# Optimization experiments

Measured on AMD Instinct MI355X. Metric: run time of the kernel, lower is better.

Reference implementation:

```python
import jax, jax.numpy as jnp
import numpy as np
import math

N_HEADS = 16
D_HEAD = 64
D_MODEL = 1024
ROPE_THETA = 10000.0


def setup_inputs() -> dict:
    key = jax.random.key(0)
    k1, k2, k3 = jax.random.split(key, 3)
    B, T = 2, 2048
    x = jax.random.normal(k1, (B, T, D_MODEL), dtype=jnp.float32)
    # torch Linear(in, out) weight has shape (out, in); store transposed (in, out)
    # so forward is x @ w. Scale like default init to keep activations sane.
    w_qkv = jax.random.normal(k2, (D_MODEL, 3 * D_MODEL), dtype=jnp.float32) / math.sqrt(D_MODEL)
    w_o = jax.random.normal(k3, (D_MODEL, D_MODEL), dtype=jnp.float32) / math.sqrt(D_MODEL)
    return {"x": x, "w_qkv": w_qkv, "w_o": w_o}


def _build_rope(T, dtype):
    inv_freq = 1.0 / (ROPE_THETA ** (jnp.arange(0, D_HEAD, 2, dtype=jnp.float32) / D_HEAD))
    t = jnp.arange(T, dtype=jnp.float32)
    freqs = jnp.outer(t, inv_freq)            # [T, D_HEAD/2]
    emb = jnp.concatenate([freqs, freqs], -1)  # [T, D_HEAD]
    return jnp.cos(emb).astype(dtype), jnp.sin(emb).astype(dtype)


def _apply_rope(x, cos, sin):
    # x: [B, T, H, D_HEAD]; cos/sin broadcast as [1, T, 1, D_HEAD]
    x1, x2 = jnp.split(x, 2, axis=-1)
    rotated = jnp.concatenate([-x2, x1], axis=-1)
    return x * cos + rotated * sin


def reference(x, w_qkv, w_o):
    B, T, D = x.shape
    qkv = (x @ w_qkv).reshape(B, T, 3, N_HEADS, D_HEAD)
    q, k, v = qkv[:, :, 0], qkv[:, :, 1], qkv[:, :, 2]  # [B, T, H, Dh]
    cos, sin = _build_rope(T, x.dtype)
    cos = cos[None, :, None, :]
    sin = sin[None, :, None, :]
    q = _apply_rope(q, cos, sin)
    k = _apply_rope(k, cos, sin)
    scale = 1.0 / math.sqrt(D_HEAD)
    # full [B, H, T, T] scores (faithful to the manual matmul-softmax-matmul)
    attn = jnp.einsum("bthd,bshd->bhts", q, k) * scale
    attn = jax.nn.softmax(attn, axis=-1)
    out = jnp.einsum("bhts,bshd->bthd", attn, v).reshape(B, T, D)
    return out @ w_o
```

## Files before the change

kernel.cpp:

```cpp
#include <hip/hip_runtime.h>
#include <cstdint>

typedef unsigned short ushort_t;
typedef __attribute__((ext_vector_type(8))) short v8s;
typedef __attribute__((ext_vector_type(4))) short v4s;
typedef __attribute__((ext_vector_type(2))) unsigned v2u;
typedef __attribute__((ext_vector_type(4))) float v4f;

#define MFMA(a, b, c) __builtin_amdgcn_mfma_f32_16x16x32_bf16(a, b, c, 0, 0, 0)
#define QSCALE 0.18033688011112042f

#define GLL(gp, lp) __builtin_amdgcn_global_load_lds(                        \
    (const __attribute__((address_space(1))) void*)(gp),                     \
    (__attribute__((address_space(3))) void*)(lp), 16, 0, 0)

#define WAIT_LGKM0() __builtin_amdgcn_s_waitcnt(0xc07f)

__device__ __forceinline__ float bf2f(ushort_t u) {
    union { unsigned u; float f; } x; x.u = ((unsigned)u) << 16; return x.f;
}
__device__ __forceinline__ short f2bf(float f) {
    union { float f; unsigned u; } x; x.f = f;
    unsigned r = x.u + 0x7fffu + ((x.u >> 16) & 1u);
    return (short)(r >> 16);
}

__global__ __launch_bounds__(256) void prep(const void* __restrict__ xin,
                                            const void* __restrict__ w1,
                                            const void* __restrict__ w2,
                                            ushort_t* __restrict__ xb,
                                            ushort_t* __restrict__ out1,
                                            ushort_t* __restrict__ out2,
                                            int* __restrict__ flag,
                                            float* __restrict__ tab) {
    __shared__ ushort_t tile[64][65];
    __shared__ int cnt;
    int bid = blockIdx.x, tid = threadIdx.x;

    int isbf = 0;
    if (bid < 3072 || bid == 3328) {
        if (tid == 0) cnt = 0;
        __syncthreads();
        unsigned w = ((const unsigned*)xin)[tid];
        int e = (w >> 7) & 0xFF;
        int hit = ((e >= 96 && e <= 135) || (w & 0xFFFFu) == 0) ? 1 : 0;
        atomicAdd(&cnt, hit);
        __syncthreads();
        isbf = (cnt >= 160) ? 1 : 0;
        if (bid == 3328) {
            if (tid == 0) *flag = isbf;
            return;
        }
    }

    if (bid < 2048) {
        int i = bid * 256 + tid;
        if (isbf) {
            ((v8s*)xb)[i] = ((const v8s*)xin)[i];
        } else {
            const float* xf = (const float*)xin + (size_t)i * 8;
            v8s o;
            #pragma unroll
            for (int j = 0; j < 8; ++j) o[j] = f2bf(xf[j]);
            ((v8s*)xb)[i] = o;
        }
    } else if (bid < 3072) {
        int t = bid - 2048;
        int bxl = t & 63, by = (t >> 6) * 64;
        const void* in; ushort_t* out; int C, bx;
        if (bxl < 48) { in = w1; out = out1; C = 3072; bx = bxl * 64; }
        else          { in = w2; out = out2; C = 1024; bx = (bxl - 48) * 64; }
        const int R = 1024;
        int tx = tid & 63, ty = tid >> 6;
        for (int i = ty; i < 64; i += 4) {
            size_t idx = (size_t)(by + i) * C + bx + tx;
            tile[i][tx] = isbf ? ((const ushort_t*)in)[idx]
                               : (ushort_t)f2bf(((const float*)in)[idx]);
        }
        __syncthreads();
        for (int i = ty; i < 64; i += 4) out[(size_t)(bx + i) * R + by + tx] = tile[tx][i];
    } else {
        int idx = (bid - 3072) * 256 + tid;
        int d = idx >> 11, t = idx & 2047;
        float inv_freq = __expf(-(float)d * 0.28782313662425575f);
        float ang = (float)t * inv_freq;
        float sn, cs;
        sincosf(ang, &sn, &cs);
        tab[d * 2048 + t]         = bf2f((ushort_t)f2bf(cs));
        tab[65536 + d * 2048 + t] = bf2f((ushort_t)f2bf(sn));
    }
}

template <int MODE, int BN>
__global__ __launch_bounds__(256) void gemm_bt(const ushort_t* __restrict__ A,
                                               const ushort_t* __restrict__ BT,
                                               void* __restrict__ C,
                                               const int* __restrict__ flagp,
                                               int M, int N, int K,
                                               ushort_t* __restrict__ Qp,
                                               ushort_t* __restrict__ Kp,
                                               ushort_t* __restrict__ Vp,
                                               const float* __restrict__ tab) {
    constexpr int NJ = BN / 32;
    __shared__ __align__(16) ushort_t As[2][128 * 32];
    __shared__ __align__(16) ushort_t Bs[2][BN * 32];
    int tid = threadIdx.x;
    int lane = tid & 63;
    int lr = lane & 15, lc = lane >> 4;
    int w = tid >> 6;
    int wr = (w >> 1) * 64, wc = (w & 1) * (BN / 2);

    int nx = gridDim.x;
    int orig = blockIdx.y * nx + blockIdx.x;
    int cpx = (nx * gridDim.y) >> 3;
    int swz = (orig & 7) * cpx + (orig >> 3);
    int m0 = (swz / nx) * 128, n0 = (swz % nx) * BN;

    int c0 = tid, c1 = tid + 256;
    int r0 = c0 >> 2, s0 = c0 & 3;
    int r1 = c1 >> 2, s1 = c1 & 3;

    const ushort_t* Ag0 = A + (size_t)(m0 + r0) * K + s0 * 8;
    const ushort_t* Ag1 = A + (size_t)(m0 + r1) * K + s1 * 8;
    const ushort_t* Bg0 = BT + (size_t)(n0 + r0) * K + s0 * 8;
    const ushort_t* Bg1 = BT + (size_t)(n0 + r1) * K + s1 * 8;
    const int aoff0 = w * 512;
    const int aoff1 = 2048 + w * 512;
    const int boff0 = w * 512;
    const int boff1 = 2048 + w * 512;

    v4f acc[4][NJ] = {};

    GLL(Ag0, &As[0][aoff0]);
    GLL(Ag1, &As[0][aoff1]);
    GLL(Bg0, &Bs[0][boff0]);
    if constexpr (BN == 128) GLL(Bg1, &Bs[0][boff1]);
    __syncthreads();

    int buf = 0;
    for (int kt = 0; kt < K; kt += 32) {
        if (kt + 32 < K) {
            int nb = buf ^ 1;
            GLL(Ag0 + kt + 32, &As[nb][aoff0]);
            GLL(Ag1 + kt + 32, &As[nb][aoff1]);
            GLL(Bg0 + kt + 32, &Bs[nb][boff0]);
            if constexpr (BN == 128) GLL(Bg1 + kt + 32, &Bs[nb][boff1]);
        }

        v8s af[4], bfr[NJ];
        #pragma unroll
        for (int i = 0; i < 4; ++i)
            af[i] = *(const v8s*)(&As[buf][0] + (wr + i * 16 + lr) * 32 + lc * 8);
        #pragma unroll
        for (int j = 0; j < NJ; ++j)
            bfr[j] = *(const v8s*)(&Bs[buf][0] + (wc + j * 16 + lr) * 32 + lc * 8);
        #pragma unroll
        for (int i = 0; i < 4; ++i)
            #pragma unroll
            for (int j = 0; j < NJ; ++j)
                acc[i][j] = MFMA(af[i], bfr[j], acc[i][j]);

        __syncthreads();
        buf ^= 1;
    }

    if (MODE == 1) {
        int store_f32 = (*flagp == 0);
        #pragma unroll
        for (int i = 0; i < 4; ++i)
            #pragma unroll
            for (int j = 0; j < NJ; ++j)
                #pragma unroll
                for (int r = 0; r < 4; ++r) {
                    int row = m0 + wr + i * 16 + lc * 4 + r;
                    int col = n0 + wc + j * 16 + lr;
                    if (store_f32)
                        ((float*)C)[(size_t)row * N + col] = acc[i][j][r];
                    else
                        ((ushort_t*)C)[(size_t)row * N + col] = (ushort_t)f2bf(acc[i][j][r]);
                }
    } else {
        int region = n0 >> 10;
        int h = ((n0 & 1023) + wc) >> 6;
        if (region < 2) {
            const float sc = (region == 0) ? QSCALE : 1.0f;
            ushort_t* dst = (region == 0) ? Qp : Kp;
            #pragma unroll
            for (int i = 0; i < 4; ++i)
                #pragma unroll
                for (int j = 0; j < 2; ++j) {
                    int d = j * 16 + lr;
                    int tg0 = m0 + wr + i * 16 + lc * 4;
                    int b = tg0 >> 11, tt0 = tg0 & 2047;
                    v4f cs4 = *(const v4f*)(tab + d * 2048 + tt0);
                    v4f sn4 = *(const v4f*)(tab + 65536 + d * 2048 + tt0);
                    #pragma unroll
                    for (int r = 0; r < 4; ++r) {
                        float x1 = acc[i][j][r], x2 = acc[i][(j + 2) % NJ][r];
                        size_t base = ((size_t)(b * 16 + h) * 2048 + tt0 + r) * 64 + d;
                        dst[base]      = (ushort_t)f2bf((x1 * cs4[r] - x2 * sn4[r]) * sc);
                        dst[base + 32] = (ushort_t)f2bf((x2 * cs4[r] + x1 * sn4[r]) * sc);
                    }
                }
        } else {
            #pragma unroll
            for (int i = 0; i < 4; ++i)
                #pragma unroll
                for (int j = 0; j < NJ; ++j) {
                    int d = j * 16 + lr;
                    int tg0 = m0 + wr + i * 16 + lc * 4;
                    int b = tg0 >> 11, tt = tg0 & 2047;
                    v4s pk;
                    #pragma unroll
                    for (int r = 0; r < 4; ++r) pk[r] = f2bf(acc[i][j][r]);
                    size_t base = (size_t)(b * 16 + h) * 131072 + (size_t)(tt >> 5) * 2048
                                + (size_t)d * 32 + (tt & 31);
                    *(v4s*)(Vp + base) = pk;
                }
        }
    }
}

__global__ __launch_bounds__(256) void gemm_o(const ushort_t* __restrict__ A,
                                              const ushort_t* __restrict__ BT,
                                              void* __restrict__ C,
                                              const int* __restrict__ flagp) {
    constexpr int K = 1024, N = 1024;
    __shared__ __align__(16) ushort_t As[2][128 * 64];
    __shared__ __align__(16) ushort_t Bs[2][64 * 64];
    int tid = threadIdx.x;
    int lane = tid & 63;
    int lr = lane & 15, lc = lane >> 4;
    int w = tid >> 6;
    int wr = (w >> 1) * 64, wc = (w & 1) * 32;

    int nx = gridDim.x;
    int orig = blockIdx.y * nx + blockIdx.x;
    int cpx = (nx * gridDim.y) >> 3;
    int swz = (orig & 7) * cpx + (orig >> 3);
    int m0 = (swz / nx) * 128, n0 = (swz % nx) * 64;

    const ushort_t* ag[4]; const ushort_t* bg[2];
    int al[4], bl[2];
    #pragma unroll
    for (int q = 0; q < 4; ++q) {
        int c = q * 256 + tid, r = c >> 3, p = c & 7;
        ag[q] = A + (size_t)(m0 + r) * K + ((p ^ (r & 7)) * 8);
        al[q] = (q * 256 + w * 64) * 8;
    }
    #pragma unroll
    for (int q = 0; q < 2; ++q) {
        int c = q * 256 + tid, r = c >> 3, p = c & 7;
        bg[q] = BT + (size_t)(n0 + r) * K + ((p ^ (r & 7)) * 8);
        bl[q] = (q * 256 + w * 64) * 8;
    }

    v4f acc[4][2] = {};

    #pragma unroll
    for (int q = 0; q < 4; ++q) GLL(ag[q], &As[0][al[q]]);
    #pragma unroll
    for (int q = 0; q < 2; ++q) GLL(bg[q], &Bs[0][bl[q]]);
    __syncthreads();

    int buf = 0;
    for (int t = 0; t < 16; ++t) {
        if (t + 1 < 16) {
            int kg = (t + 1) * 64, nb = buf ^ 1;
            #pragma unroll
            for (int q = 0; q < 4; ++q) GLL(ag[q] + kg, &As[nb][al[q]]);
            #pragma unroll
            for (int q = 0; q < 2; ++q) GLL(bg[q] + kg, &Bs[nb][bl[q]]);
        }

        v8s af[4][2], bf[2][2];
        #pragma unroll
        for (int i = 0; i < 4; ++i)
            #pragma unroll
            for (int kk = 0; kk < 2; ++kk)
                af[i][kk] = *(const v8s*)(&As[buf][0] + (wr + i * 16 + lr) * 64
                                          + (((kk * 4 + lc) ^ (lr & 7)) * 8));
        #pragma unroll
        for (int j = 0; j < 2; ++j)
            #pragma unroll
            for (int kk = 0; kk < 2; ++kk)
                bf[j][kk] = *(const v8s*)(&Bs[buf][0] + (wc + j * 16 + lr) * 64
                                          + (((kk * 4 + lc) ^ (lr & 7)) * 8));
        __builtin_amdgcn_s_setprio(1);
        #pragma unroll
        for (int i = 0; i < 4; ++i)
            #pragma unroll
            for (int j = 0; j < 2; ++j) {
                acc[i][j] = MFMA(af[i][0], bf[j][0], acc[i][j]);
                acc[i][j] = MFMA(af[i][1], bf[j][1], acc[i][j]);
            }
        __builtin_amdgcn_s_setprio(0);

        __syncthreads();
        buf ^= 1;
    }

    int store_f32 = (*flagp == 0);
    #pragma unroll
    for (int i = 0; i < 4; ++i)
        #pragma unroll
        for (int j = 0; j < 2; ++j)
            #pragma unroll
            for (int r = 0; r < 4; ++r) {
                int row = m0 + wr + i * 16 + lc * 4 + r;
                int col = n0 + wc + j * 16 + lr;
                if (store_f32)
                    ((float*)C)[(size_t)row * N + col] = acc[i][j][r];
                else
                    ((ushort_t*)C)[(size_t)row * N + col] = (ushort_t)f2bf(acc[i][j][r]);
            }
}

__global__ __launch_bounds__(512) void attn(const ushort_t* __restrict__ Qr,
                                            const ushort_t* __restrict__ Kr,
                                            const ushort_t* __restrict__ Vt,
                                            ushort_t* __restrict__ AO) {
    __shared__ __align__(16) char lds[65536];
    int tid = threadIdx.x, lane = tid & 63, W = tid >> 6;
    int lr = lane & 15, lc = lane >> 4;
    int qsub = W & 1, sh = W >> 1;
    int L = blockIdx.x;
    int bh = (L & 7) * 4 + ((L >> 3) & 3);
    int qt = L >> 5;
    int q0 = qt * 128 + qsub * 64;
    int b = bh >> 4, h = bh & 15;
    const ushort_t* Qb = Qr + ((size_t)bh * 2048 + q0) * 64;
    const ushort_t* Kb = Kr + (size_t)bh * 131072 + (size_t)sh * 32768;
    const ushort_t* Vb = Vt + (size_t)bh * 131072 + (size_t)sh * 32768;
    ushort_t* KsG = (ushort_t*)(lds + sh * 16384);
    ushort_t* VsG = (ushort_t*)(lds + sh * 16384 + 8192);

    int gt = tid & 127;
    int c0 = gt, c1 = gt + 128;
    int kr0 = c0 >> 3, kc0 = c0 & 7, kr1 = c1 >> 3, kc1 = c1 & 7;
    const ushort_t* Kg0 = Kb + (size_t)kr0 * 64 + kc0 * 8;
    const ushort_t* Kg1 = Kb + (size_t)kr1 * 64 + kc1 * 8;
    int kl0 = kr0 * 64 + (kc0 ^ (kr0 & 7)) * 8;
    int kl1 = kr1 * 64 + (kc1 ^ (kr1 & 7)) * 8;
    const ushort_t* Vg0 = Vb + (size_t)c0 * 8;
    const ushort_t* Vg1 = Vb + (size_t)c1 * 8;
    int vl0 = c0 * 8, vl1 = c1 * 8;

    int blr = (lr >> 2) * 8 + (lr & 3);

    v8s qf[4][2];
    #pragma unroll
    for (int jq = 0; jq < 4; ++jq)
        #pragma unroll
        for (int kk = 0; kk < 2; ++kk)
            qf[jq][kk] = *(const v8s*)(Qb + (size_t)(jq * 16 + lr) * 64 + kk * 32 + lc * 8);

    v4f o[4][4] = {};
    float li[4] = {0.f, 0.f, 0.f, 0.f};

    v8s ka = *(const v8s*)(Kg0), kb2 = *(const v8s*)(Kg1);
    v8s va = *(const v8s*)(Vg0), vb2 = *(const v8s*)(Vg1);
    *(v8s*)(KsG + kl0) = ka;
    *(v8s*)(KsG + kl1) = kb2;
    *(v8s*)(VsG + vl0) = va;
    *(v8s*)(VsG + vl1) = vb2;
    ka  = *(const v8s*)(Kg0 + 2048);
    kb2 = *(const v8s*)(Kg1 + 2048);
    va  = *(const v8s*)(Vg0 + 2048);
    vb2 = *(const v8s*)(Vg1 + 2048);
    __syncthreads();

    #pragma unroll 1
    for (int t = 0; t < 16; ++t) {
        int p = t & 1;
        const ushort_t* Kl = KsG + p * 2048;
        const ushort_t* Vl = VsG + p * 2048;

        v8s kf[2][2], vf[4];
        #pragma unroll
        for (int hh = 0; hh < 2; ++hh) {
            int rn = blr + hh * 4;
            int sw = hh * 4 + (lr & 3);
            #pragma unroll
            for (int kk = 0; kk < 2; ++kk)
                kf[hh][kk] = *(const v8s*)(Kl + rn * 64 + (((kk * 4 + lc) ^ sw) * 8));
        }
        #pragma unroll
        for (int i = 0; i < 4; ++i)
            vf[i] = *(const v8s*)(Vl + (i * 16 + lr) * 32 + lc * 8);

        v4f St[2][4] = {};
        __builtin_amdgcn_s_setprio(1);
        #pragma unroll
        for (int hh = 0; hh < 2; ++hh)
            #pragma unroll
            for (int jq = 0; jq < 4; ++jq) {
                St[hh][jq] = MFMA(kf[hh][0], qf[jq][0], St[hh][jq]);
                St[hh][jq] = MFMA(kf[hh][1], qf[jq][1], St[hh][jq]);
            }
        __builtin_amdgcn_s_setprio(0);

        if (t + 1 < 16) {
            ushort_t* Kn = KsG + (p ^ 1) * 2048;
            ushort_t* Vn = VsG + (p ^ 1) * 2048;
            *(v8s*)(Kn + kl0) = ka;
            *(v8s*)(Kn + kl1) = kb2;
            *(v8s*)(Vn + vl0) = va;
            *(v8s*)(Vn + vl1) = vb2;
        }
        if (t + 2 < 16) {
            ka  = *(const v8s*)(Kg0 + (size_t)(t + 2) * 2048);
            kb2 = *(const v8s*)(Kg1 + (size_t)(t + 2) * 2048);
            va  = *(const v8s*)(Vg0 + (size_t)(t + 2) * 2048);
            vb2 = *(const v8s*)(Vg1 + (size_t)(t + 2) * 2048);
        }

        v8s pf[4];
        #pragma unroll
        for (int jq = 0; jq < 4; ++jq) {
            union { unsigned u[4]; v8s v; } P;
            #pragma unroll
            for (int hh = 0; hh < 2; ++hh) {
                #pragma unroll
                for (int r = 0; r < 4; ++r) {
                    float ev = __builtin_amdgcn_exp2f(St[hh][jq][r]);
                    St[hh][jq][r] = ev;
                    li[jq] += ev;
                }
                P.u[hh * 2 + 0] = __builtin_amdgcn_perm(__float_as_uint(St[hh][jq][1]),
                                                        __float_as_uint(St[hh][jq][0]), 0x07060302u);
                P.u[hh * 2 + 1] = __builtin_amdgcn_perm(__float_as_uint(St[hh][jq][3]),
                                                        __float_as_uint(St[hh][jq][2]), 0x07060302u);
            }
            pf[jq] = P.v;
        }
        __builtin_amdgcn_s_setprio(1);
        #pragma unroll
        for (int jq = 0; jq < 4; ++jq)
            #pragma unroll
            for (int i = 0; i < 4; ++i)
                o[i][jq] = MFMA(vf[i], pf[jq], o[i][jq]);
        __builtin_amdgcn_s_setprio(0);
        WAIT_LGKM0();
        __builtin_amdgcn_s_barrier();
    }

    #pragma unroll
    for (int jq = 0; jq < 4; ++jq) {
        li[jq] += __shfl_xor(li[jq], 16);
        li[jq] += __shfl_xor(li[jq], 32);
    }

    float* MO = (float*)lds;
    float* Ml = (float*)(lds + 52224);
    __syncthreads();
    #pragma unroll 1
    for (int ph = 0; ph < 2; ++ph) {
        if (qsub == ph && sh != 0) {
            float* M = MO + (sh - 1) * 4352;
            #pragma unroll
            for (int jq = 0; jq < 4; ++jq) {
                #pragma unroll
                for (int i = 0; i < 4; ++i)
                    *(v4f*)(M + (jq * 16 + lr) * 68 + i * 16 + lc * 4) = o[i][jq];
                if (lc == 0) Ml[(sh - 1) * 64 + jq * 16 + lr] = li[jq];
            }
        }
        __syncthreads();
        if (qsub == ph && sh == 0) {
            #pragma unroll
            for (int jq = 0; jq < 4; ++jq) {
                int row = jq * 16 + lr;
                float ls = li[jq] + Ml[row] + Ml[64 + row] + Ml[128 + row];
                float inv = 1.0f / ls;
                int tq = q0 + row;
                #pragma unroll
                for (int i = 0; i < 4; ++i) {
                    v4f m0v = *(const v4f*)(MO + row * 68 + i * 16 + lc * 4);
                    v4f m1v = *(const v4f*)(MO + 4352 + row * 68 + i * 16 + lc * 4);
                    v4f m2v = *(const v4f*)(MO + 8704 + row * 68 + i * 16 + lc * 4);
                    v4s pk;
                    #pragma unroll
                    for (int r = 0; r < 4; ++r)
                        pk[r] = f2bf((o[i][jq][r] + m0v[r] + m1v[r] + m2v[r]) * inv);
                    *(v4s*)(AO + (size_t)(b * 2048 + tq) * 1024 + h * 64 + i * 16 + lc * 4) = pk;
                }
            }
        }
        __syncthreads();
    }
}

extern "C" void kernel_launch(void* const* d_in, const int* in_sizes, int n_in,
                              void* d_out, int out_size, void* d_ws, size_t ws_size,
                              hipStream_t stream) {
    char* ws = (char*)d_ws;
    int*      flag  = (int*)ws;
    ushort_t* wqkvT = (ushort_t*)(ws + 256);
    ushort_t* woT   = (ushort_t*)(ws + 6291712);
    ushort_t* xb    = (ushort_t*)(ws + 8388864);
    ushort_t* Qr    = (ushort_t*)(ws + 16777472);
    ushort_t* Kr    = (ushort_t*)(ws + 25166080);
    ushort_t* Vt    = (ushort_t*)(ws + 33554688);
    ushort_t* AO    = (ushort_t*)(ws + 41943296);
    float*    tab   = (float*)(ws + 50331904);

    prep<<<3329, 256, 0, stream>>>(d_in[0], d_in[1], d_in[2], xb, wqkvT, woT, flag, tab);
    gemm_bt<2, 128><<<dim3(24, 32), 256, 0, stream>>>(xb, wqkvT, nullptr, flag, 4096, 3072, 1024,
                                                      Qr, Kr, Vt, tab);
    attn<<<512, 512, 0, stream>>>(Qr, Kr, Vt, AO);
    gemm_o<<<dim3(16, 32), 256, 0, stream>>>(AO, woT, d_out, flag);
}
```

Baseline: 187.2 us.

## Load V fragments directly from global in attention; shrink output GEMM tile

Attention no longer stages V tiles through LDS. Each wave reads its V fragments directly from global memory every iteration, which cuts LDS use and removes the LDS store/load traffic for V. The output projection GEMM now uses 64x64 tiles with twice as many blocks and a higher occupancy launch bound. The risks are exposed global-load latency for V, since it is no longer prefetched, and less reuse per block in the GEMM.

```diff
diff --git a/kernel.cpp b/kernel.cpp
--- a/kernel.cpp
+++ b/kernel.cpp
@@ -221,46 +221,41 @@
     }
 }
 
-__global__ __launch_bounds__(256) void gemm_o(const ushort_t* __restrict__ A,
-                                              const ushort_t* __restrict__ BT,
-                                              void* __restrict__ C,
-                                              const int* __restrict__ flagp) {
+__global__ __launch_bounds__(256, 4) void gemm_o(const ushort_t* __restrict__ A,
+                                                 const ushort_t* __restrict__ BT,
+                                                 void* __restrict__ C,
+                                                 const int* __restrict__ flagp) {
     constexpr int K = 1024, N = 1024;
-    __shared__ __align__(16) ushort_t As[2][128 * 64];
+    __shared__ __align__(16) ushort_t As[2][64 * 64];
     __shared__ __align__(16) ushort_t Bs[2][64 * 64];
     int tid = threadIdx.x;
     int lane = tid & 63;
     int lr = lane & 15, lc = lane >> 4;
     int w = tid >> 6;
-    int wr = (w >> 1) * 64, wc = (w & 1) * 32;
+    int wr = (w >> 1) * 32, wc = (w & 1) * 32;
 
     int nx = gridDim.x;
     int orig = blockIdx.y * nx + blockIdx.x;
     int cpx = (nx * gridDim.y) >> 3;
     int swz = (orig & 7) * cpx + (orig >> 3);
-    int m0 = (swz / nx) * 128, n0 = (swz % nx) * 64;
-
-    const ushort_t* ag[4]; const ushort_t* bg[2];
-    int al[4], bl[2];
-    #pragma unroll
-    for (int q = 0; q < 4; ++q) {
+    int m0 = (swz / nx) * 64, n0 = (swz % nx) * 64;
+
+    const ushort_t* ag[2]; const ushort_t* bg[2];
+    int lof[2];
+    #pragma unroll
+    for (int q = 0; q < 2; ++q) {
         int c = q * 256 + tid, r = c >> 3, p = c & 7;
         ag[q] = A + (size_t)(m0 + r) * K + ((p ^ (r & 7)) * 8);
-        al[q] = (q * 256 + w * 64) * 8;
-    }
-    #pragma unroll
-    for (int q = 0; q < 2; ++q) {
-        int c = q * 256 + tid, r = c >> 3, p = c & 7;
         bg[q] = BT + (size_t)(n0 + r) * K + ((p ^ (r & 7)) * 8);
-        bl[q] = (q * 256 + w * 64) * 8;
-    }
-
-    v4f acc[4][2] = {};
-
-    #pragma unroll
-    for (int q = 0; q < 4; ++q) GLL(ag[q], &As[0][al[q]]);
-    #pragma unroll
-    for (int q = 0; q < 2; ++q) GLL(bg[q], &Bs[0][bl[q]]);
+        lof[q] = (q * 256 + w * 64) * 8;
+    }
+
+    v4f acc[2][2] = {};
+
+    #pragma unroll
+    for (int q = 0; q < 2; ++q) GLL(ag[q], &As[0][lof[q]]);
+    #pragma unroll
+    for (int q = 0; q < 2; ++q) GLL(bg[q], &Bs[0][lof[q]]);
     __syncthreads();
 
     int buf = 0;
@@ -268,14 +263,14 @@
         if (t + 1 < 16) {
             int kg = (t + 1) * 64, nb = buf ^ 1;
             #pragma unroll
-            for (int q = 0; q < 4; ++q) GLL(ag[q] + kg, &As[nb][al[q]]);
-            #pragma unroll
-            for (int q = 0; q < 2; ++q) GLL(bg[q] + kg, &Bs[nb][bl[q]]);
-        }
-
-        v8s af[4][2], bf[2][2];
-        #pragma unroll
-        for (int i = 0; i < 4; ++i)
+            for (int q = 0; q < 2; ++q) GLL(ag[q] + kg, &As[nb][lof[q]]);
+            #pragma unroll
+            for (int q = 0; q < 2; ++q) GLL(bg[q] + kg, &Bs[nb][lof[q]]);
+        }
+
+        v8s af[2][2], bf[2][2];
+        #pragma unroll
+        for (int i = 0; i < 2; ++i)
             #pragma unroll
             for (int kk = 0; kk < 2; ++kk)
                 af[i][kk] = *(const v8s*)(&As[buf][0] + (wr + i * 16 + lr) * 64
@@ -288,7 +283,7 @@
                                           + (((kk * 4 + lc) ^ (lr & 7)) * 8));
         __builtin_amdgcn_s_setprio(1);
         #pragma unroll
-        for (int i = 0; i < 4; ++i)
+        for (int i = 0; i < 2; ++i)
             #pragma unroll
             for (int j = 0; j < 2; ++j) {
                 acc[i][j] = MFMA(af[i][0], bf[j][0], acc[i][j]);
@@ -302,7 +297,7 @@
 
     int store_f32 = (*flagp == 0);
     #pragma unroll
-    for (int i = 0; i < 4; ++i)
+    for (int i = 0; i < 2; ++i)
         #pragma unroll
         for (int j = 0; j < 2; ++j)
             #pragma unroll
@@ -320,7 +315,7 @@
                                             const ushort_t* __restrict__ Kr,
                                             const ushort_t* __restrict__ Vt,
                                             ushort_t* __restrict__ AO) {
-    __shared__ __align__(16) char lds[65536];
+    __shared__ __align__(16) char lds[53248];
     int tid = threadIdx.x, lane = tid & 63, W = tid >> 6;
     int lr = lane & 15, lc = lane >> 4;
     int qsub = W & 1, sh = W >> 1;
@@ -332,8 +327,7 @@
     const ushort_t* Qb = Qr + ((size_t)bh * 2048 + q0) * 64;
     const ushort_t* Kb = Kr + (size_t)bh * 131072 + (size_t)sh * 32768;
     const ushort_t* Vb = Vt + (size_t)bh * 131072 + (size_t)sh * 32768;
-    ushort_t* KsG = (ushort_t*)(lds + sh * 16384);
-    ushort_t* VsG = (ushort_t*)(lds + sh * 16384 + 8192);
+    ushort_t* KsG = (ushort_t*)(lds + sh * 8192);
 
     int gt = tid & 127;
     int c0 = gt, c1 = gt + 128;
@@ -342,9 +336,6 @@
     const ushort_t* Kg1 = Kb + (size_t)kr1 * 64 + kc1 * 8;
     int kl0 = kr0 * 64 + (kc0 ^ (kr0 & 7)) * 8;
     int kl1 = kr1 * 64 + (kc1 ^ (kr1 & 7)) * 8;
-    const ushort_t* Vg0 = Vb + (size_t)c0 * 8;
-    const ushort_t* Vg1 = Vb + (size_t)c1 * 8;
-    int vl0 = c0 * 8, vl1 = c1 * 8;
 
     int blr = (lr >> 2) * 8 + (lr & 3);
 
@@ -359,24 +350,24 @@
     float li[4] = {0.f, 0.f, 0.f, 0.f};
 
     v8s ka = *(const v8s*)(Kg0), kb2 = *(const v8s*)(Kg1);
-    v8s va = *(const v8s*)(Vg0), vb2 = *(const v8s*)(Vg1);
     *(v8s*)(KsG + kl0) = ka;
     *(v8s*)(KsG + kl1) = kb2;
-    *(v8s*)(VsG + vl0) = va;
-    *(v8s*)(VsG + vl1) = vb2;
     ka  = *(const v8s*)(Kg0 + 2048);
     kb2 = *(const v8s*)(Kg1 + 2048);
-    va  = *(const v8s*)(Vg0 + 2048);
-    vb2 = *(const v8s*)(Vg1 + 2048);
     __syncthreads();
 
     #pragma unroll 1
     for (int t = 0; t < 16; ++t) {
         int p = t & 1;
         const ushort_t* Kl = KsG + p * 2048;
-        const ushort_t* Vl = VsG + p * 2048;
-
-        v8s kf[2][2], vf[4];
+        const ushort_t* Vg = Vb + (size_t)t * 2048;
+
+        v8s vf[4];
+        #pragma unroll
+        for (int i = 0; i < 4; ++i)
+            vf[i] = *(const v8s*)(Vg + (i * 16 + lr) * 32 + lc * 8);
+
+        v8s kf[2][2];
         #pragma unroll
         for (int hh = 0; hh < 2; ++hh) {
             int rn = blr + hh * 4;
@@ -385,9 +376,6 @@
             for (int kk = 0; kk < 2; ++kk)
                 kf[hh][kk] = *(const v8s*)(Kl + rn * 64 + (((kk * 4 + lc) ^ sw) * 8));
         }
-        #pragma unroll
-        for (int i = 0; i < 4; ++i)
-            vf[i] = *(const v8s*)(Vl + (i * 16 + lr) * 32 + lc * 8);
 
         v4f St[2][4] = {};
         __builtin_amdgcn_s_setprio(1);
@@ -402,17 +390,12 @@
 
         if (t + 1 < 16) {
             ushort_t* Kn = KsG + (p ^ 1) * 2048;
-            ushort_t* Vn = VsG + (p ^ 1) * 2048;
             *(v8s*)(Kn + kl0) = ka;
             *(v8s*)(Kn + kl1) = kb2;
-            *(v8s*)(Vn + vl0) = va;
-            *(v8s*)(Vn + vl1) = vb2;
         }
         if (t + 2 < 16) {
             ka  = *(const v8s*)(Kg0 + (size_t)(t + 2) * 2048);
             kb2 = *(const v8s*)(Kg1 + (size_t)(t + 2) * 2048);
-            va  = *(const v8s*)(Vg0 + (size_t)(t + 2) * 2048);
-            vb2 = *(const v8s*)(Vg1 + (size_t)(t + 2) * 2048);
         }
 
         v8s pf[4];
@@ -509,5 +492,5 @@
     gemm_bt<2, 128><<<dim3(24, 32), 256, 0, stream>>>(xb, wqkvT, nullptr, flag, 4096, 3072, 1024,
                                                       Qr, Kr, Vt, tab);
     attn<<<512, 512, 0, stream>>>(Qr, Kr, Vt, AO);
-    gemm_o<<<dim3(16, 32), 256, 0, stream>>>(AO, woT, d_out, flag);
-}
+    gemm_o<<<dim3(16, 64), 256, 0, stream>>>(AO, woT, d_out, flag);
+}
```

New measurement: 186.6 us. Within noise of the previous version (-0.3%).
